# Optimization experiments

Hardware: AMD Instinct MI355X
Metric: run time of the kernel (lower is better)

Reference implementation:

```python
import jax, jax.numpy as jnp
import numpy as np

B, T, IN, H, OUT = 64, 512, 512, 1024, 1


def _uniform(key, shape, stdv):
    return jax.random.uniform(key, shape, jnp.float32, -stdv, stdv)


def setup_inputs() -> dict:
    key = jax.random.key(0)
    ks = jax.random.split(key, 12)
    stdv = 1.0 / H ** 0.5
    x = jax.random.normal(ks[0], (B, T, IN), jnp.float32)
    # layer 0 cell (input_size=IN), layer 1 cell (input_size=H)
    w_ih0 = _uniform(ks[1], (4 * H, IN), stdv)
    w_hh0 = _uniform(ks[2], (4 * H, H), stdv)
    b_ih0 = _uniform(ks[3], (4 * H,), stdv)
    b_hh0 = _uniform(ks[4], (4 * H,), stdv)
    w_ih1 = _uniform(ks[5], (4 * H, H), stdv)
    w_hh1 = _uniform(ks[6], (4 * H, H), stdv)
    b_ih1 = _uniform(ks[7], (4 * H,), stdv)
    b_hh1 = _uniform(ks[8], (4 * H,), stdv)
    # nn.Linear default init: U(-1/sqrt(fan_in), 1/sqrt(fan_in))
    s_out = 1.0 / H ** 0.5
    w_out = _uniform(ks[9], (OUT, H), s_out)
    b_out = _uniform(ks[10], (OUT,), s_out)
    return dict(x=x, w_ih0=w_ih0, w_hh0=w_hh0, b_ih0=b_ih0, b_hh0=b_hh0,
                w_ih1=w_ih1, w_hh1=w_hh1, b_ih1=b_ih1, b_hh1=b_hh1,
                w_out=w_out, b_out=b_out)


def _lstm_layer(x_tbi, w_ih, w_hh, b_ih, b_hh):
    # x_tbi: [T, B, in]. Batch the input-to-hidden GEMM over all timesteps.
    gx = jnp.einsum('tbi,gi->tbg', x_tbi, w_ih) + b_ih + b_hh  # [T,B,4H]

    def step(carry, gxt):
        h, c = carry
        gates = gxt + h @ w_hh.T  # [B,4H]
        i, f, g, o = jnp.split(gates, 4, axis=1)
        c = jax.nn.sigmoid(f) * c + jax.nn.sigmoid(i) * jnp.tanh(g)
        h = jax.nn.sigmoid(o) * jnp.tanh(c)
        return (h, c), h

    h0 = jnp.zeros((x_tbi.shape[1], w_hh.shape[1]), x_tbi.dtype)
    (_, _), hs = jax.lax.scan(step, (h0, h0), gx)
    return hs  # [T,B,H]


def reference(x, w_ih0, w_hh0, b_ih0, b_hh0, w_ih1, w_hh1, b_ih1, b_hh1, w_out, b_out):
    xt = jnp.transpose(x, (1, 0, 2))  # [T,B,IN] (batch_first)
    h1 = _lstm_layer(xt, w_ih0, w_hh0, b_ih0, b_hh0)
    h2 = _lstm_layer(h1, w_ih1, w_hh1, b_ih1, b_hh1)
    out = jnp.einsum('tbh,oh->tbo', h2, w_out) + b_out  # [T,B,OUT]
    return jnp.transpose(out, (1, 0, 2))  # [B,T,OUT]
```

## Files before the change

kernel.cpp:

```cpp
#include <hip/hip_runtime.h>

#define T_SEQ 512
#define B_SZ  64
#define IN_SZ 512
#define H_SZ  1024
#define NBLK  256
#define NTHR  512

#define FLG_STRIDE 4
#define FLG_ROW    (128 * FLG_STRIDE)

typedef _Float16 f16;
typedef _Float16 half8 __attribute__((ext_vector_type(8)));
typedef float    f32x4 __attribute__((ext_vector_type(4)));

#define SM_WFRAG 0
#define SM_PART  131072
#define SM_C     (131072 + 16384)
#define SM_BIAS  (131072 + 16384 + 2048)
#define SM_STAGE (131072 + 16384 + 2048 + 128)
#define SMEM_BYTES (131072 + 16384 + 2048 + 128 + 1024)

struct Params {
    const float *x;
    const float *wih0, *whh0, *bih0, *bhh0;
    const float *wih1, *whh1, *bih1, *bhh1;
    f16 *h1all;
    f16 *h2all;
    int *flg0, *flg1;
};

__device__ __forceinline__ float sigf(float x)     { return 1.f / (1.f + __expf(-x)); }
__device__ __forceinline__ float tanhfast(float x) { return 2.f / (1.f + __expf(-2.f * x)) - 1.f; }

__global__ __launch_bounds__(NTHR, 2) void persist_kernel(Params p)
{
    extern __shared__ char smem[];
    f16*   wfrag = (f16*)(smem + SM_WFRAG);
    float* P     = (float*)(smem + SM_PART);
    float* c_lds = (float*)(smem + SM_C);
    float* bl    = (float*)(smem + SM_BIAS);
    f16*   hst   = (f16*)(smem + SM_STAGE);

    const int tid = threadIdx.x;
    const int l   = tid & 63, wv = tid >> 6;
    const int n16 = l & 15,  q  = l >> 4;
    const int mt  = wv & 3,  kp = wv >> 2;
    const int layer = blockIdx.x >> 7;
    const int bid   = blockIdx.x & 127;
    const int jb    = bid * 8;

    {
        const int gate0 = n16 >> 3, c8 = n16 & 7;
        const int nfrag = layer ? 128 : 96;
        for (int f = wv; f < nfrag; f += 8) {
            int kstep = f >> 1, nt = f & 1;
            int wrow = (nt * 2 + gate0) * H_SZ + jb + c8;
            const float* src;
            if (layer == 0) {
                src = (kstep < 16) ? p.wih0 + (size_t)wrow * IN_SZ + kstep * 32 + q * 8
                                   : p.whh0 + (size_t)wrow * H_SZ + (kstep - 16) * 32 + q * 8;
            } else {
                src = (kstep < 32) ? p.wih1 + (size_t)wrow * H_SZ + kstep * 32 + q * 8
                                   : p.whh1 + (size_t)wrow * H_SZ + (kstep - 32) * 32 + q * 8;
            }
            half8 hv;
            #pragma unroll
            for (int u = 0; u < 8; ++u) hv[u] = (f16)src[u];
            *(half8*)(wfrag + f * 512 + l * 8) = hv;
        }
        if (tid < 32) {
            int gate = tid >> 3, col = tid & 7;
            int wrow = gate * H_SZ + jb + col;
            bl[tid] = layer ? (p.bih1[wrow] + p.bhh1[wrow])
                            : (p.bih0[wrow] + p.bhh0[wrow]);
        }
        c_lds[tid] = 0.f;
    }
    __syncthreads();

    auto ldB = [&](int kg, int nt) -> half8 {
        return *(const half8*)(wfrag + (kg * 2 + nt) * 512 + l * 8);
    };
    auto pollAll = [&](const int* fl) {
        const int* a0 = fl + l * FLG_STRIDE;
        const int* a1 = fl + (l + 64) * FLG_STRIDE;
        while (true) {
            int va = __hip_atomic_load(a0, __ATOMIC_RELAXED, __HIP_MEMORY_SCOPE_AGENT);
            int vb = __hip_atomic_load(a1, __ATOMIC_RELAXED, __HIP_MEMORY_SCOPE_AGENT);
            if (__all(va & vb)) break;
            __builtin_amdgcn_s_sleep(1);
        }
    };
    auto finish = [&](int s, const f32x4& acc0, const f32x4& acc1,
                      f16* dstAll, int* myflg) {
        int slot = kp * 8 + mt * 2;
        *(f32x4*)(P + (slot + 0) * 256 + l * 4) = acc0;
        *(f32x4*)(P + (slot + 1) * 256 + l * 4) = acc1;
        __syncthreads();
        {
            int b = tid >> 3, col = tid & 7;
            int bmt = b >> 4, r = b & 15;
            int base = (r >> 2) * 64 + (r & 3);
            int s0 = (bmt * 2 + 0) * 256 + base;
            int s1 = (bmt * 2 + 1) * 256 + base;
            float iv = P[s0 + col * 4]        + P[s0 + 2048 + col * 4]        + bl[col];
            float fv = P[s0 + (col + 8) * 4]  + P[s0 + 2048 + (col + 8) * 4]  + bl[8 + col];
            float gv = P[s1 + col * 4]        + P[s1 + 2048 + col * 4]        + bl[16 + col];
            float ov = P[s1 + (col + 8) * 4]  + P[s1 + 2048 + (col + 8) * 4]  + bl[24 + col];
            float co = c_lds[tid];
            float ii = sigf(iv), ff = sigf(fv), gg = tanhfast(gv), oo = sigf(ov);
            float cn = ff * co + ii * gg;
            float hn = oo * tanhfast(cn);
            c_lds[tid] = cn;
            hst[b * 8 + col] = (f16)hn;
        }
        __syncthreads();
        if (tid < 128) {
            int b = tid >> 1, half = tid & 1;
            unsigned long long v = *(const unsigned long long*)(hst + b * 8 + half * 4);
            f16* dst = dstAll + (size_t)s * (B_SZ * H_SZ);
            __hip_atomic_store((unsigned long long*)(dst + (size_t)b * H_SZ + jb + half * 4), v,
                               __ATOMIC_RELAXED, __HIP_MEMORY_SCOPE_AGENT);
        }
        __syncthreads();
        if (tid == 0)
            __hip_atomic_store(myflg + (size_t)s * FLG_ROW + bid * FLG_STRIDE, 1,
                               __ATOMIC_RELAXED, __HIP_MEMORY_SCOPE_AGENT);
    };

    if (layer == 0) {
        half8 brx0[8], brx1[8], brr0[16], brr1[16];
        #pragma unroll
        for (int u = 0; u < 8; ++u)  { int kg = kp * 8 + u;       brx0[u] = ldB(kg, 0); brx1[u] = ldB(kg, 1); }
        #pragma unroll
        for (int u = 0; u < 16; ++u) { int kg = 16 + kp * 16 + u; brr0[u] = ldB(kg, 0); brr1[u] = ldB(kg, 1); }

        for (int s = 0; s < T_SEQ; ++s) {
            f32x4 acc0 = {}, acc1 = {};
            #pragma unroll
            for (int u = 0; u < 8; ++u) {
                int kb = (kp * 8 + u) * 32 + q * 8;
                const float* ap = p.x + ((size_t)(mt * 16 + n16) * T_SEQ + s) * IN_SZ + kb;
                f32x4 xa = *(const f32x4*)ap;
                f32x4 xb = *(const f32x4*)(ap + 4);
                half8 af;
                #pragma unroll
                for (int u2 = 0; u2 < 4; ++u2) { af[u2] = (f16)xa[u2]; af[4 + u2] = (f16)xb[u2]; }
                acc0 = __builtin_amdgcn_mfma_f32_16x16x32_f16(af, brx0[u], acc0, 0, 0, 0);
                acc1 = __builtin_amdgcn_mfma_f32_16x16x32_f16(af, brx1[u], acc1, 0, 0, 0);
            }
            if (s > 0) {
                if (wv == 0) pollAll(p.flg0 + (size_t)(s - 1) * FLG_ROW);
                __syncthreads();
                const f16* hp = p.h1all + (size_t)(s - 1) * (B_SZ * H_SZ)
                              + (size_t)(mt * 16 + n16) * H_SZ + kp * 512 + q * 8;
                #pragma unroll
                for (int u = 0; u < 16; ++u) {
                    half8 af = *(const half8*)(hp + u * 32);
                    acc0 = __builtin_amdgcn_mfma_f32_16x16x32_f16(af, brr0[u], acc0, 0, 0, 0);
                    acc1 = __builtin_amdgcn_mfma_f32_16x16x32_f16(af, brr1[u], acc1, 0, 0, 0);
                }
            }
            finish(s, acc0, acc1, p.h1all, p.flg0);
        }
    } else {
        half8 bri0[16], bri1[16], brr0[8], brr1[8];
        #pragma unroll
        for (int u = 0; u < 16; ++u) { int kg = kp * 16 + u;      bri0[u] = ldB(kg, 0); bri1[u] = ldB(kg, 1); }
        #pragma unroll
        for (int u = 0; u < 8; ++u)  { int kg = 32 + kp * 16 + u; brr0[u] = ldB(kg, 0); brr1[u] = ldB(kg, 1); }

        for (int s = 0; s < T_SEQ; ++s) {
            f32x4 acc0 = {}, acc1 = {};
            if (s > 0) {
                if (wv == 0) pollAll(p.flg1 + (size_t)(s - 1) * FLG_ROW);
                __syncthreads();
                const f16* hp = p.h2all + (size_t)(s - 1) * (B_SZ * H_SZ)
                              + (size_t)(mt * 16 + n16) * H_SZ + kp * 512 + q * 8;
                #pragma unroll
                for (int u = 0; u < 8; ++u) {
                    half8 af = *(const half8*)(hp + u * 32);
                    acc0 = __builtin_amdgcn_mfma_f32_16x16x32_f16(af, brr0[u], acc0, 0, 0, 0);
                    acc1 = __builtin_amdgcn_mfma_f32_16x16x32_f16(af, brr1[u], acc1, 0, 0, 0);
                }
                #pragma unroll
                for (int u = 8; u < 16; ++u) {
                    int kg = 32 + kp * 16 + u;
                    half8 b0 = ldB(kg, 0), b1 = ldB(kg, 1);
                    half8 af = *(const half8*)(hp + u * 32);
                    acc0 = __builtin_amdgcn_mfma_f32_16x16x32_f16(af, b0, acc0, 0, 0, 0);
                    acc1 = __builtin_amdgcn_mfma_f32_16x16x32_f16(af, b1, acc1, 0, 0, 0);
                }
            }
            if (wv == 0) pollAll(p.flg0 + (size_t)s * FLG_ROW);
            __syncthreads();
            {
                const f16* hp = p.h1all + (size_t)s * (B_SZ * H_SZ)
                              + (size_t)(mt * 16 + n16) * H_SZ + kp * 512 + q * 8;
                #pragma unroll
                for (int u = 0; u < 16; ++u) {
                    half8 af = *(const half8*)(hp + u * 32);
                    acc0 = __builtin_amdgcn_mfma_f32_16x16x32_f16(af, bri0[u], acc0, 0, 0, 0);
                    acc1 = __builtin_amdgcn_mfma_f32_16x16x32_f16(af, bri1[u], acc1, 0, 0, 0);
                }
            }
            finish(s, acc0, acc1, p.h2all, p.flg1);
        }
    }
}

__global__ __launch_bounds__(256) void gemv_kernel(
    const f16* __restrict__ h2all, const float* __restrict__ wout,
    const float* __restrict__ bout, float* __restrict__ out)
{
    int t = blockIdx.x;
    int wave = threadIdx.x >> 6, lane = threadIdx.x & 63;
    float w[16];
    #pragma unroll
    for (int u = 0; u < 16; ++u) w[u] = wout[lane * 16 + u];
    float b0 = bout[0];
    for (int b = wave; b < B_SZ; b += 4) {
        const f16* hp = h2all + ((size_t)t * B_SZ + b) * H_SZ + lane * 16;
        float sum = 0.f;
        #pragma unroll
        for (int u = 0; u < 16; ++u) sum += (float)hp[u] * w[u];
        #pragma unroll
        for (int off = 32; off; off >>= 1) sum += __shfl_down(sum, off, 64);
        if (lane == 0) out[(size_t)b * T_SEQ + t] = sum + b0;
    }
}

extern "C" void kernel_launch(void* const* d_in, const int* in_sizes, int n_in,
                              void* d_out, int out_size, void* d_ws, size_t ws_size,
                              hipStream_t stream)
{
    const float* x    = (const float*)d_in[0];
    const float* wih0 = (const float*)d_in[1];
    const float* whh0 = (const float*)d_in[2];
    const float* bih0 = (const float*)d_in[3];
    const float* bhh0 = (const float*)d_in[4];
    const float* wih1 = (const float*)d_in[5];
    const float* whh1 = (const float*)d_in[6];
    const float* bih1 = (const float*)d_in[7];
    const float* bhh1 = (const float*)d_in[8];
    const float* wout = (const float*)d_in[9];
    const float* bout = (const float*)d_in[10];
    float* out = (float*)d_out;

    char* ws = (char*)d_ws;
    size_t off = 0;
    auto alloc = [&](size_t bytes) -> void* {
        void* pp = ws + off;
        off += (bytes + 255) & ~(size_t)255;
        return pp;
    };
    f16* h1all = (f16*)alloc((size_t)T_SEQ * B_SZ * H_SZ * 2);
    f16* h2all = (f16*)alloc((size_t)T_SEQ * B_SZ * H_SZ * 2);
    const size_t flg_bytes = (size_t)2 * T_SEQ * FLG_ROW * 4;
    int* flgs  = (int*)alloc(flg_bytes);

    (void)hipMemsetAsync(flgs, 0, flg_bytes, stream);

    Params pa;
    pa.x = x;
    pa.wih0 = wih0; pa.whh0 = whh0; pa.bih0 = bih0; pa.bhh0 = bhh0;
    pa.wih1 = wih1; pa.whh1 = whh1; pa.bih1 = bih1; pa.bhh1 = bhh1;
    pa.h1all = h1all; pa.h2all = h2all;
    pa.flg0 = flgs; pa.flg1 = flgs + T_SEQ * FLG_ROW;

    (void)hipFuncSetAttribute((const void*)persist_kernel,
                              hipFuncAttributeMaxDynamicSharedMemorySize, SMEM_BYTES);

    hipStreamCaptureStatus cap = hipStreamCaptureStatusNone;
    (void)hipStreamIsCapturing(stream, &cap);
    bool launched = false;
    if (cap == hipStreamCaptureStatusNone) {
        void* kargs[] = { (void*)&pa };
        if (hipLaunchCooperativeKernel((const void*)persist_kernel, dim3(NBLK), dim3(NTHR),
                                       kargs, SMEM_BYTES, stream) == hipSuccess)
            launched = true;
    }
    if (!launched)
        persist_kernel<<<NBLK, NTHR, SMEM_BYTES, stream>>>(pa);

    gemv_kernel<<<T_SEQ, 256, 0, stream>>>(h2all, wout, bout, out);
}
```

Measured before the change: 4.973 ms.

## Make every wave poll flags, prefetch next x-GEMM, and streamline h publish

Each wave now polls the step flags itself instead of wave 0 polling and then a block-wide barrier, and layer 1 waits on both dependency rows in a single combined poll. The layer-0 input projection for step s+1 is computed right after finishing step s, so it sits off the critical path that waits on the recurrent flag. The h store is done by one wave with the flag written using release ordering, which drops a barrier. This adds more atomic polling traffic from all waves, and the ordering now depends on the release semantics applying to the same wave's stores.

After: 8.451 ms. 69.9% more time.

```diff
diff --git a/kernel.cpp b/kernel.cpp
--- a/kernel.cpp
+++ b/kernel.cpp
@@ -13,6 +13,7 @@
 typedef _Float16 f16;
 typedef _Float16 half8 __attribute__((ext_vector_type(8)));
 typedef float    f32x4 __attribute__((ext_vector_type(4)));
+typedef unsigned long long ull;
 
 #define SM_WFRAG 0
 #define SM_PART  131072
@@ -82,13 +83,27 @@
     auto ldB = [&](int kg, int nt) -> half8 {
         return *(const half8*)(wfrag + (kg * 2 + nt) * 512 + l * 8);
     };
-    auto pollAll = [&](const int* fl) {
+    auto pollRow = [&](const int* fl) {
         const int* a0 = fl + l * FLG_STRIDE;
         const int* a1 = fl + (l + 64) * FLG_STRIDE;
         while (true) {
             int va = __hip_atomic_load(a0, __ATOMIC_RELAXED, __HIP_MEMORY_SCOPE_AGENT);
             int vb = __hip_atomic_load(a1, __ATOMIC_RELAXED, __HIP_MEMORY_SCOPE_AGENT);
             if (__all(va & vb)) break;
+            __builtin_amdgcn_s_sleep(1);
+        }
+    };
+    auto pollTwo = [&](const int* fA, const int* fB) {
+        const int* a0 = fA + l * FLG_STRIDE;
+        const int* a1 = fA + (l + 64) * FLG_STRIDE;
+        const int* b0 = fB + l * FLG_STRIDE;
+        const int* b1 = fB + (l + 64) * FLG_STRIDE;
+        while (true) {
+            int va = __hip_atomic_load(a0, __ATOMIC_RELAXED, __HIP_MEMORY_SCOPE_AGENT);
+            int vb = __hip_atomic_load(a1, __ATOMIC_RELAXED, __HIP_MEMORY_SCOPE_AGENT);
+            int vc = __hip_atomic_load(b0, __ATOMIC_RELAXED, __HIP_MEMORY_SCOPE_AGENT);
+            int vd = __hip_atomic_load(b1, __ATOMIC_RELAXED, __HIP_MEMORY_SCOPE_AGENT);
+            if (__all(va & vb & vc & vd)) break;
             __builtin_amdgcn_s_sleep(1);
         }
     };
@@ -116,17 +131,16 @@
             hst[b * 8 + col] = (f16)hn;
         }
         __syncthreads();
-        if (tid < 128) {
-            int b = tid >> 1, half = tid & 1;
-            unsigned long long v = *(const unsigned long long*)(hst + b * 8 + half * 4);
-            f16* dst = dstAll + (size_t)s * (B_SZ * H_SZ);
-            __hip_atomic_store((unsigned long long*)(dst + (size_t)b * H_SZ + jb + half * 4), v,
-                               __ATOMIC_RELAXED, __HIP_MEMORY_SCOPE_AGENT);
-        }
-        __syncthreads();
-        if (tid == 0)
-            __hip_atomic_store(myflg + (size_t)s * FLG_ROW + bid * FLG_STRIDE, 1,
-                               __ATOMIC_RELAXED, __HIP_MEMORY_SCOPE_AGENT);
+        if (wv == 0) {
+            f16* dst = dstAll + (size_t)s * (B_SZ * H_SZ) + (size_t)l * H_SZ + jb;
+            ull v0 = *(const ull*)(hst + l * 8);
+            ull v1 = *(const ull*)(hst + l * 8 + 4);
+            __hip_atomic_store((ull*)(dst + 0), v0, __ATOMIC_RELAXED, __HIP_MEMORY_SCOPE_AGENT);
+            __hip_atomic_store((ull*)(dst + 4), v1, __ATOMIC_RELAXED, __HIP_MEMORY_SCOPE_AGENT);
+            if (l == 0)
+                __hip_atomic_store(myflg + (size_t)s * FLG_ROW + bid * FLG_STRIDE, 1,
+                                   __ATOMIC_RELEASE, __HIP_MEMORY_SCOPE_AGENT);
+        }
     };
 
     if (layer == 0) {
@@ -136,8 +150,7 @@
         #pragma unroll
         for (int u = 0; u < 16; ++u) { int kg = 16 + kp * 16 + u; brr0[u] = ldB(kg, 0); brr1[u] = ldB(kg, 1); }
 
-        for (int s = 0; s < T_SEQ; ++s) {
-            f32x4 acc0 = {}, acc1 = {};
+        auto x_gemm = [&](int s, f32x4& a0, f32x4& a1) {
             #pragma unroll
             for (int u = 0; u < 8; ++u) {
                 int kb = (kp * 8 + u) * 32 + q * 8;
@@ -147,12 +160,18 @@
                 half8 af;
                 #pragma unroll
                 for (int u2 = 0; u2 < 4; ++u2) { af[u2] = (f16)xa[u2]; af[4 + u2] = (f16)xb[u2]; }
-                acc0 = __builtin_amdgcn_mfma_f32_16x16x32_f16(af, brx0[u], acc0, 0, 0, 0);
-                acc1 = __builtin_amdgcn_mfma_f32_16x16x32_f16(af, brx1[u], acc1, 0, 0, 0);
-            }
+                a0 = __builtin_amdgcn_mfma_f32_16x16x32_f16(af, brx0[u], a0, 0, 0, 0);
+                a1 = __builtin_amdgcn_mfma_f32_16x16x32_f16(af, brx1[u], a1, 0, 0, 0);
+            }
+        };
+
+        f32x4 xacc0 = {}, xacc1 = {};
+        x_gemm(0, xacc0, xacc1);
+
+        for (int s = 0; s < T_SEQ; ++s) {
+            f32x4 acc0 = xacc0, acc1 = xacc1;
             if (s > 0) {
-                if (wv == 0) pollAll(p.flg0 + (size_t)(s - 1) * FLG_ROW);
-                __syncthreads();
+                pollRow(p.flg0 + (size_t)(s - 1) * FLG_ROW);
                 const f16* hp = p.h1all + (size_t)(s - 1) * (B_SZ * H_SZ)
                               + (size_t)(mt * 16 + n16) * H_SZ + kp * 512 + q * 8;
                 #pragma unroll
@@ -163,6 +182,10 @@
                 }
             }
             finish(s, acc0, acc1, p.h1all, p.flg0);
+            if (s + 1 < T_SEQ) {
+                xacc0 = (f32x4){}; xacc1 = (f32x4){};
+                x_gemm(s + 1, xacc0, xacc1);
+            }
         }
     } else {
         half8 bri0[16], bri1[16], brr0[8], brr1[8];
@@ -173,9 +196,10 @@
 
         for (int s = 0; s < T_SEQ; ++s) {
             f32x4 acc0 = {}, acc1 = {};
+            if (s == 0) pollRow(p.flg0);
+            else pollTwo(p.flg0 + (size_t)s * FLG_ROW, p.flg1 + (size_t)(s - 1) * FLG_ROW);
+
             if (s > 0) {
-                if (wv == 0) pollAll(p.flg1 + (size_t)(s - 1) * FLG_ROW);
-                __syncthreads();
                 const f16* hp = p.h2all + (size_t)(s - 1) * (B_SZ * H_SZ)
                               + (size_t)(mt * 16 + n16) * H_SZ + kp * 512 + q * 8;
                 #pragma unroll
@@ -193,8 +217,6 @@
                     acc1 = __builtin_amdgcn_mfma_f32_16x16x32_f16(af, b1, acc1, 0, 0, 0);
                 }
             }
-            if (wv == 0) pollAll(p.flg0 + (size_t)s * FLG_ROW);
-            __syncthreads();
             {
                 const f16* hp = p.h1all + (size_t)s * (B_SZ * H_SZ)
                               + (size_t)(mt * 16 + n16) * H_SZ + kp * 512 + q * 8;
```
